# Performance work log

Hardware: AMD Instinct MI355X
Metric: run time of the kernel (lower is better)

Reference implementation:

```python
import jax, jax.numpy as jnp
import numpy as np

N = 64          # truth table size (2^6)
NUM_VARS = 6
TOP_K = 16
BATCH = 524288
IN_DIM = 17 + TOP_K  # 33
HID = 64
OUT = 64
EPS_LN = 1e-5


def _hadamard(n: int) -> np.ndarray:
    H = np.array([[1.0]], dtype=np.float32)
    while H.shape[0] < n:
        H = np.block([[H, H], [H, -H]])
    return H

_HAMMING = np.array([bin(i).count('1') for i in range(N)], dtype=np.float32)


def _xavier(key, fan_in, fan_out):
    lim = np.sqrt(6.0 / (fan_in + fan_out)).astype(np.float32)
    return jax.random.uniform(key, (fan_in, fan_out), jnp.float32, -lim, lim)


def setup_inputs() -> dict:
    key = jax.random.key(0)
    ks = jax.random.split(key, 4)
    truth_table = jax.random.randint(ks[0], (BATCH, N), 0, 2).astype(jnp.int32)
    H = jnp.asarray(_hadamard(N))
    return {
        'truth_table': truth_table,
        'H': H,
        'W1': _xavier(ks[1], IN_DIM, HID), 'b1': jnp.zeros((HID,), jnp.float32),
        'g1': jnp.ones((HID,), jnp.float32), 'be1': jnp.zeros((HID,), jnp.float32),
        'W2': _xavier(ks[2], HID, HID), 'b2': jnp.zeros((HID,), jnp.float32),
        'g2': jnp.ones((HID,), jnp.float32), 'be2': jnp.zeros((HID,), jnp.float32),
        'W3': _xavier(ks[3], HID, OUT), 'b3': jnp.zeros((OUT,), jnp.float32),
    }


def _layernorm(x, g, b):
    m = jnp.mean(x, axis=-1, keepdims=True)
    v = jnp.mean((x - m) ** 2, axis=-1, keepdims=True)
    return (x - m) / jnp.sqrt(v + EPS_LN) * g + b


def _walsh_features(truth_table, H):
    # Walsh-Hadamard transform: torch.mm(H, f.T).T == f @ H.T == f @ H (H symmetric)
    f_polar = 1.0 - 2.0 * truth_table.astype(jnp.float32)  # [B, 64]
    walsh = f_polar @ H                                     # [B, 64]
    walsh_abs = jnp.abs(walsh)
    walsh_sq = walsh * walsh
    n = jnp.float32(N)

    # --- key coefficients (8d): W(0), W(2^i) i=0..5, W(n-1) ---
    key_idx = jnp.array([0, 1, 2, 4, 8, 16, 32, N - 1])
    key_coeffs = walsh[:, key_idx] / n                      # [B, 8]

    # --- spectral statistics (5d) ---
    threshold = 0.1 * n
    sparsity = jnp.mean((walsh_abs < threshold).astype(jnp.float32), axis=1, keepdims=True)
    max_abs = jnp.max(walsh_abs, axis=1, keepdims=True)
    max_mag = max_abs / n
    l1 = jnp.sum(walsh_abs, axis=1, keepdims=True) / (n * n)
    sumsq = jnp.sum(walsh_sq, axis=1, keepdims=True)
    l2 = jnp.sqrt(sumsq) / (n * n)
    p = walsh_sq / (sumsq + 1e-10)
    entropy = -jnp.sum(p * jnp.log(p + 1e-10), axis=1, keepdims=True) / jnp.log(n)
    spectral = jnp.concatenate([sparsity, max_mag, l1, l2, entropy], axis=1)  # [B, 5]

    # --- linearity indicators (4d) ---
    large_coeffs = jnp.sum((walsh_abs > 0.5 * n).astype(jnp.float32), axis=1, keepdims=True)
    is_linear = ((large_coeffs >= 1) & (large_coeffs <= 2)).astype(jnp.float32)
    nonlinearity = jnp.clip(0.5 - max_abs / (2 * n), 0.0, 0.5) * 2.0
    hw = jnp.asarray(_HAMMING)
    large_mask = (walsh_abs > threshold).astype(jnp.float32)
    degree = jnp.sum(large_mask * hw, axis=1, keepdims=True) / (
        jnp.sum(large_mask, axis=1, keepdims=True) + 1e-10) / NUM_VARS
    bent_mag = jnp.float32(2.0 ** (NUM_VARS / 2))  # 8.0
    bent_dev = jnp.mean(jnp.abs(walsh_abs - bent_mag) / bent_mag, axis=1, keepdims=True)
    is_bent = (bent_dev < 0.1).astype(jnp.float32)
    linearity = jnp.concatenate([is_linear, nonlinearity, degree, is_bent], axis=1)  # [B, 4]

    # --- top-k |W| coefficients (16d) ---
    topk = jax.lax.top_k(walsh_abs, TOP_K)[0] / n            # [B, 16]

    return jnp.concatenate([key_coeffs, spectral, linearity, topk], axis=1)  # [B, 33]


def reference(truth_table, H, W1, b1, g1, be1, W2, b2, g2, be2, W3, b3):
    feats = _walsh_features(truth_table, H)
    h = jax.nn.gelu(_layernorm(feats @ W1 + b1, g1, be1), approximate=False)
    # Dropout(0.1) is identity in eval mode
    h = jax.nn.gelu(_layernorm(h @ W2 + b2, g2, be2), approximate=False)
    return h @ W3 + b3  # [B, 64]
```

## Files before the change

kernel.cpp:

```cpp
#include <hip/hip_runtime.h>
#include <math.h>

#define TPB 256

typedef _Float16 half8 __attribute__((ext_vector_type(8)));
typedef _Float16 h2 __attribute__((ext_vector_type(2)));
typedef float f32x4 __attribute__((ext_vector_type(4)));

__device__ __forceinline__ int swz(int row, int col) {
    return row * 64 + ((((col >> 3) ^ row) & 7) << 3) + (col & 7);
}

__device__ __forceinline__ unsigned int pk_f16(float a, float b) {
    auto p = __builtin_amdgcn_cvt_pkrtz(a, b);
    return __builtin_bit_cast(unsigned int, p);
}

__device__ __forceinline__ float gelu_sig(float x) {
    float t = fmaf(0.1029433247f, x * x, 2.3022089899f);
    float e = __builtin_amdgcn_exp2f(-x * t);
    return x * __builtin_amdgcn_rcpf(1.0f + e);
}

__device__ __forceinline__ void ce2(h2& x, h2& y) {
    h2 mx = __builtin_elementwise_max(x, y);
    h2 mn = __builtin_elementwise_min(x, y);
    x = mx; y = mn;
}

template<int CTRL>
__device__ __forceinline__ f32x4 dpp_add4(f32x4 x) {
#pragma unroll
    for (int r = 0; r < 4; ++r) {
        int o = __builtin_amdgcn_update_dpp(0, __float_as_int(x[r]),
                                            CTRL, 0xf, 0xf, false);
        x[r] += __int_as_float(o);
    }
    return x;
}
__device__ __forceinline__ f32x4 row_reduce16(f32x4 x) {
    x = dpp_add4<0x121>(x);
    x = dpp_add4<0x122>(x);
    x = dpp_add4<0x124>(x);
    x = dpp_add4<0x128>(x);
    return x;
}

__global__ void weight_stage_kernel(const float* __restrict__ W1,
                                    const float* __restrict__ W2,
                                    const float* __restrict__ W3,
                                    _Float16* __restrict__ wsW) {
    const int idx = blockIdx.x * 256 + threadIdx.x;
    if (idx >= 3 * 4 * 2 * 64 * 8) return;
    const int e    = idx & 7;
    const int lane = (idx >> 3) & 63;
    const int s    = (idx >> 9) & 1;
    const int nt   = (idx >> 10) & 3;
    const int L    = idx >> 12;
    const int g = lane >> 4, i = lane & 15;
    const int k = 32 * s + 8 * g + e;
    const int n = 4 * i + nt;
    const float* W = (L == 0) ? W1 : (L == 1) ? W2 : W3;
    const int K = (L == 0) ? 33 : 64;
    float val = (k < K) ? W[k * 64 + n] : 0.0f;
    if (L == 0 && (k < 8 || (k >= 17 && k < 33))) val *= 0.015625f;
    const _Float16 hi = (_Float16)val;
    const size_t base = ((((size_t)L * 4 + nt) * 2 + s) * 2) * 512
                        + (size_t)lane * 8 + e;
    wsW[base]       = hi;
    wsW[base + 512] = (_Float16)(val - (float)hi);
}

template<bool LAST>
__device__ __forceinline__ void mfma_layer(
    _Float16* actB,
    const _Float16* __restrict__ wsL,
    const float* __restrict__ bias, const float* __restrict__ gg,
    const float* __restrict__ bb,
    float* outp, int rowbase, int nrows)
{
    const int l = threadIdx.x & 63;
    const int g = l >> 4, i = l & 15;

    const half8* Bp = reinterpret_cast<const half8*>(wsL);
    half8 Bh[4][2], Bl[4][2];
#pragma unroll
    for (int nt = 0; nt < 4; ++nt) {
#pragma unroll
        for (int s = 0; s < 2; ++s) {
            Bh[nt][s] = Bp[((nt * 2 + s) * 2 + 0) * 64 + l];
            Bl[nt][s] = Bp[((nt * 2 + s) * 2 + 1) * 64 + l];
        }
    }
    const f32x4 bvv = *(const f32x4*)&bias[4 * i];
    f32x4 gvv, bevv;
    if (!LAST) {
        gvv  = *(const f32x4*)&gg[4 * i];
        bevv = *(const f32x4*)&bb[4 * i];
    }
    const bool full = LAST && (rowbase + 63 < nrows);

    half8 A0 = *(const half8*)&actB[swz(i, 8 * g)];
    half8 A1 = *(const half8*)&actB[swz(i, 32 + 8 * g)];

#pragma unroll
    for (int t = 0; t < 4; ++t) {
        half8 nA0, nA1;
        if (t < 3) {
            nA0 = *(const half8*)&actB[swz(16 * (t + 1) + i, 8 * g)];
            nA1 = *(const half8*)&actB[swz(16 * (t + 1) + i, 32 + 8 * g)];
        }
        f32x4 D[4];
#pragma unroll
        for (int nt = 0; nt < 4; ++nt) {
            f32x4 d = {bvv[nt], bvv[nt], bvv[nt], bvv[nt]};
            d = __builtin_amdgcn_mfma_f32_16x16x32_f16(A0, Bh[nt][0], d, 0, 0, 0);
            d = __builtin_amdgcn_mfma_f32_16x16x32_f16(A1, Bh[nt][1], d, 0, 0, 0);
            d = __builtin_amdgcn_mfma_f32_16x16x32_f16(A0, Bl[nt][0], d, 0, 0, 0);
            d = __builtin_amdgcn_mfma_f32_16x16x32_f16(A1, Bl[nt][1], d, 0, 0, 0);
            D[nt] = d;
        }
        if (LAST) {
#pragma unroll
            for (int r = 0; r < 4; ++r) {
                const int grow = rowbase + 16 * t + 4 * g + r;
                if (full || grow < nrows) {
                    f32x4 st = {D[0][r], D[1][r], D[2][r], D[3][r]};
                    *reinterpret_cast<f32x4*>(&outp[(size_t)grow * 64 + 4 * i]) = st;
                }
            }
        } else {
            f32x4 s4 = (D[0] + D[1]) + (D[2] + D[3]);
            f32x4 q4 = D[0] * D[0];
            q4 = D[1] * D[1] + q4;
            q4 = D[2] * D[2] + q4;
            q4 = D[3] * D[3] + q4;
            s4 = row_reduce16(s4);
            q4 = row_reduce16(q4);
            f32x4 mean = s4 * 0.015625f;
            f32x4 rstd, mr;
#pragma unroll
            for (int r = 0; r < 4; ++r) {
                float var = q4[r] * 0.015625f - mean[r] * mean[r];
                rstd[r] = rsqrtf(var + 1e-5f);
                mr[r] = -mean[r] * rstd[r];
            }
#pragma unroll
            for (int r = 0; r < 4; ++r) {
                float x0 = fmaf(fmaf(D[0][r], rstd[r], mr[r]), gvv[0], bevv[0]);
                float x1 = fmaf(fmaf(D[1][r], rstd[r], mr[r]), gvv[1], bevv[1]);
                float x2 = fmaf(fmaf(D[2][r], rstd[r], mr[r]), gvv[2], bevv[2]);
                float x3 = fmaf(fmaf(D[3][r], rstd[r], mr[r]), gvv[3], bevv[3]);
                uint2 st;
                st.x = pk_f16(gelu_sig(x0), gelu_sig(x1));
                st.y = pk_f16(gelu_sig(x2), gelu_sig(x3));
                *reinterpret_cast<uint2*>(
                    &actB[swz(16 * t + 4 * g + r, 4 * i)]) = st;
            }
        }
        if (t < 3) { A0 = nA0; A1 = nA1; }
    }
    if (!LAST) asm volatile("s_waitcnt lgkmcnt(0)" ::: "memory");
}

__global__ __launch_bounds__(TPB, 2) void walsh_mlp_kernel(
    const int* __restrict__ tt,
    const float* __restrict__ b1,
    const float* __restrict__ g1, const float* __restrict__ be1,
    const float* __restrict__ b2,
    const float* __restrict__ g2, const float* __restrict__ be2,
    const float* __restrict__ b3,
    const _Float16* __restrict__ wsW,
    float* __restrict__ out, int nrows)
{
    __shared__ __align__(16) _Float16 sAct[4][64][64];

    const int tid = threadIdx.x;
    const int w = tid >> 6, l = tid & 63;
    _Float16* actB = &sAct[w][0][0];

    const int row = blockIdx.x * TPB + tid;
    const int rowc = (row < nrows) ? row : (nrows - 1);

    int4 raw[16];
    const int4* t4 = reinterpret_cast<const int4*>(tt + (size_t)rowc * 64);
#pragma unroll
    for (int q = 0; q < 16; ++q) raw[q] = t4[q];

    {
        float* lut = reinterpret_cast<float*>(actB);
        if (l < 33) {
            const float a = 2.0f * (float)l;
            const float pq = (a * a) * 2.44140625e-4f;
            lut[l] = -(pq * __logf(pq + 1e-10f));
        }
    }
    asm volatile("s_waitcnt lgkmcnt(0)" ::: "memory");

    h2 p[32];
#pragma unroll
    for (int q = 0; q < 8; ++q) {
        int4 alo = raw[q];
        int4 ahi = raw[q + 8];
        p[4 * q + 0] = __builtin_bit_cast(h2,
            0x3C003C00u | ((unsigned)alo.x << 15) | ((unsigned)ahi.x << 31));
        p[4 * q + 1] = __builtin_bit_cast(h2,
            0x3C003C00u | ((unsigned)alo.y << 15) | ((unsigned)ahi.y << 31));
        p[4 * q + 2] = __builtin_bit_cast(h2,
            0x3C003C00u | ((unsigned)alo.z << 15) | ((unsigned)ahi.z << 31));
        p[4 * q + 3] = __builtin_bit_cast(h2,
            0x3C003C00u | ((unsigned)alo.w << 15) | ((unsigned)ahi.w << 31));
    }

#pragma unroll
    for (int h = 1; h < 32; h <<= 1) {
#pragma unroll
        for (int i = 0; i < 32; ++i) {
            if ((i & h) == 0) {
                h2 a = p[i], b = p[i | h];
                p[i] = a + b;
                p[i | h] = a - b;
            }
        }
    }

    const float inv_n = 1.0f / 64.0f;
    const float* lutr = reinterpret_cast<const float*>(actB);
    float f[17];
    h2 habs[32];
    const h2 kONE  = {(_Float16)1.0f, (_Float16)1.0f};
    const h2 kZERO = {(_Float16)0.0f, (_Float16)0.0f};
    const h2 k64   = {(_Float16)64.0f, (_Float16)64.0f};
    const h2 kCsp  = {(_Float16)409.5f, (_Float16)409.5f};
    const h2 kClg  = {(_Float16)-2080.0f, (_Float16)-2080.0f};
    const h2 kM8   = {(_Float16)-8.0f, (_Float16)-8.0f};
    h2 sum2 = kZERO, max2 = kZERO, bent2 = kZERO;
    h2 csp2 = kZERO, clg2 = kZERO, chw2 = kZERO;
    float ent = 0.0f;
#pragma unroll
    for (int i = 0; i < 32; ++i) {
        const float lo = (float)p[i][0], hi = (float)p[i][1];
        const float a0 = lo + hi;
        const float a1 = lo - hi;
        if (i == 0)  { f[0] = a0; f[6] = a1; }
        if (i == 1)  f[1] = a0;
        if (i == 2)  f[2] = a0;
        if (i == 4)  f[3] = a0;
        if (i == 8)  f[4] = a0;
        if (i == 16) f[5] = a0;
        if (i == 31) f[7] = a1;
        const h2 a = __builtin_bit_cast(h2, pk_f16(a0, a1) & 0x7FFF7FFFu);
        habs[i] = a;
        sum2 = sum2 + a;
        max2 = __builtin_elementwise_max(max2, a);
        bent2 = bent2 + __builtin_bit_cast(h2,
            __builtin_bit_cast(unsigned, a + kM8) & 0x7FFF7FFFu);
        const h2 ssp = __builtin_elementwise_min(kONE,
            __builtin_elementwise_max(kZERO, kCsp - a * k64));
        csp2 = csp2 + ssp;
        clg2 = clg2 + __builtin_elementwise_min(kONE,
            __builtin_elementwise_max(kZERO, a * k64 + kClg));
        const float PC = (float)__builtin_popcount(i);
        const h2 hp = {(_Float16)PC, (_Float16)PC};
        chw2 = chw2 + (kONE - ssp) * hp;
        ent += lutr[((int)fabsf(a0)) >> 1];
        ent += lutr[((int)fabsf(a1)) >> 1];
    }
    const float sumabs = (float)sum2[0] + (float)sum2[1];
    const float maxab  = fmaxf((float)max2[0], (float)max2[1]);
    const float bent   = (float)bent2[0] + (float)bent2[1];
    const float cnt_sp = (float)csp2[0] + (float)csp2[1];
    const float cnt_lg = (float)clg2[0] + (float)clg2[1];
    const float sum_hw = (float)chw2[0] + (float)chw2[1]
                       + (32.0f - (float)csp2[1]);

    f[8]  = cnt_sp * inv_n;
    f[9]  = maxab * inv_n;
    f[10] = sumabs * (1.0f / 4096.0f);
    f[11] = 0.015625f;
    f[12] = ent * 0.24044917348149316f;
    f[13] = (cnt_lg >= 0.5f && cnt_lg <= 2.5f) ? 1.0f : 0.0f;
    f[14] = fmaxf(0.0f, 0.5f - maxab * (1.0f / 128.0f)) * 2.0f;
    f[15] = sum_hw / (64.0f - cnt_sp + 1e-10f) * (1.0f / 6.0f);
    f[16] = (bent < 51.2f) ? 1.0f : 0.0f;

    h2 t2[16];
    {
#pragma unroll
        for (int base = 0; base < 32; base += 16) {
#pragma unroll
            for (int pp = 1; pp < 16; pp <<= 1) {
#pragma unroll
                for (int k = pp; k >= 1; k >>= 1) {
#pragma unroll
                    for (int j = k & (pp - 1); j + k < 16; j += 2 * k) {
#pragma unroll
                        for (int i = 0; i < k; ++i) {
                            if (i + j + k < 16 &&
                                (i + j) / (2 * pp) == (i + j + k) / (2 * pp))
                                ce2(habs[base + i + j], habs[base + i + j + k]);
                        }
                    }
                }
            }
        }
        h2 mm[16];
#pragma unroll
        for (int i = 0; i < 16; ++i)
            mm[i] = __builtin_elementwise_max(habs[i], habs[31 - i]);
#pragma unroll
        for (int d = 8; d >= 1; d >>= 1) {
#pragma unroll
            for (int i = 0; i < 16; ++i)
                if ((i & d) == 0) ce2(mm[i], mm[i + d]);
        }
#pragma unroll
        for (int i = 0; i < 16; ++i) {
            unsigned m = __builtin_bit_cast(unsigned, mm[15 - i]);
            unsigned sw = __builtin_amdgcn_alignbit(m, m, 16);
            t2[i] = __builtin_elementwise_max(mm[i], __builtin_bit_cast(h2, sw));
        }
#pragma unroll
        for (int d = 8; d >= 1; d >>= 1) {
#pragma unroll
            for (int i = 0; i < 16; ++i)
                if ((i & d) == 0) ce2(t2[i], t2[i + d]);
        }
    }

    {
        unsigned wd[32];
#pragma unroll
        for (int j = 0; j < 8; ++j) wd[j] = pk_f16(f[2 * j], f[2 * j + 1]);
        {
            unsigned lo = (unsigned)__builtin_bit_cast(unsigned short,
                                                       (_Float16)f[16]);
            wd[8] = lo | (__builtin_bit_cast(unsigned, t2[0]) << 16);
        }
#pragma unroll
        for (int m = 0; m < 7; ++m)
            wd[9 + m] = (__builtin_bit_cast(unsigned, t2[2 * m + 1]) & 0xFFFFu)
                      | (__builtin_bit_cast(unsigned, t2[2 * m + 2]) << 16);
        wd[16] = __builtin_bit_cast(unsigned, t2[15]) & 0xFFFFu;
#pragma unroll
        for (int j = 17; j < 32; ++j) wd[j] = 0u;
#pragma unroll
        for (int c = 0; c < 8; ++c) {
            uint4 st;
            st.x = wd[4 * c + 0]; st.y = wd[4 * c + 1];
            st.z = wd[4 * c + 2]; st.w = wd[4 * c + 3];
            *reinterpret_cast<uint4*>(&actB[swz(l, c * 8)]) = st;
        }
    }
    asm volatile("s_waitcnt lgkmcnt(0)" ::: "memory");

    const int rowbase = blockIdx.x * TPB + w * 64;
    mfma_layer<false>(actB, wsW,         b1, g1, be1, nullptr, 0, 0);
    mfma_layer<false>(actB, wsW + 8192,  b2, g2, be2, nullptr, 0, 0);
    mfma_layer<true >(actB, wsW + 16384, b3, nullptr, nullptr,
                      out, rowbase, nrows);
}

extern "C" void kernel_launch(void* const* d_in, const int* in_sizes, int n_in,
                              void* d_out, int out_size, void* d_ws, size_t ws_size,
                              hipStream_t stream) {
    const int*   tt  = (const int*)d_in[0];
    const float* W1  = (const float*)d_in[2];
    const float* b1  = (const float*)d_in[3];
    const float* g1  = (const float*)d_in[4];
    const float* be1 = (const float*)d_in[5];
    const float* W2  = (const float*)d_in[6];
    const float* b2  = (const float*)d_in[7];
    const float* g2  = (const float*)d_in[8];
    const float* be2 = (const float*)d_in[9];
    const float* W3  = (const float*)d_in[10];
    const float* b3  = (const float*)d_in[11];
    float* out = (float*)d_out;
    _Float16* wsW = (_Float16*)d_ws;

    const int nrows = in_sizes[0] / 64;

    hipLaunchKernelGGL(weight_stage_kernel, dim3(48), dim3(256), 0, stream,
                       W1, W2, W3, wsW);

    const int grid = (nrows + TPB - 1) / TPB;
    hipLaunchKernelGGL(walsh_mlp_kernel, dim3(grid), dim3(TPB), 0, stream,
                       tt, b1, g1, be1, b2, g2, be2, b3, wsW, out, nrows);
}
```

Measured before the change: 90.95 us.

## Use single-wave blocks, prefetch layer-1 weights, raise MFMA priority, interleave sort

Shrinks blocks from four waves to one, so each block uses a single 64x64 shared tile and the waves schedule independently. Loads the layer-1 high-half weight fragments early, before the feature store, to hide their global latency. Wraps the MFMA sequence in s_setprio to favour matrix issue, and interleaves the two 16-element sorting networks so there is more instruction-level parallelism. The risks are more blocks to launch and higher register pressure from the prefetched fragments.

Measured after the change: 86.88 us. -4.5%, faster.

```diff
diff --git a/kernel.cpp b/kernel.cpp
--- a/kernel.cpp
+++ b/kernel.cpp
@@ -1,7 +1,7 @@
 #include <hip/hip_runtime.h>
 #include <math.h>
 
-#define TPB 256
+#define TPB 64
 
 typedef _Float16 half8 __attribute__((ext_vector_type(8)));
 typedef _Float16 h2 __attribute__((ext_vector_type(2)));
@@ -75,6 +75,7 @@
 __device__ __forceinline__ void mfma_layer(
     _Float16* actB,
     const _Float16* __restrict__ wsL,
+    const half8 (*Bh_pre)[2],
     const float* __restrict__ bias, const float* __restrict__ gg,
     const float* __restrict__ bb,
     float* outp, int rowbase, int nrows)
@@ -88,7 +89,8 @@
     for (int nt = 0; nt < 4; ++nt) {
 #pragma unroll
         for (int s = 0; s < 2; ++s) {
-            Bh[nt][s] = Bp[((nt * 2 + s) * 2 + 0) * 64 + l];
+            Bh[nt][s] = Bh_pre ? Bh_pre[nt][s]
+                               : Bp[((nt * 2 + s) * 2 + 0) * 64 + l];
             Bl[nt][s] = Bp[((nt * 2 + s) * 2 + 1) * 64 + l];
         }
     }
@@ -111,6 +113,7 @@
             nA1 = *(const half8*)&actB[swz(16 * (t + 1) + i, 32 + 8 * g)];
         }
         f32x4 D[4];
+        __builtin_amdgcn_s_setprio(1);
 #pragma unroll
         for (int nt = 0; nt < 4; ++nt) {
             f32x4 d = {bvv[nt], bvv[nt], bvv[nt], bvv[nt]};
@@ -120,6 +123,7 @@
             d = __builtin_amdgcn_mfma_f32_16x16x32_f16(A1, Bl[nt][1], d, 0, 0, 0);
             D[nt] = d;
         }
+        __builtin_amdgcn_s_setprio(0);
         if (LAST) {
 #pragma unroll
             for (int r = 0; r < 4; ++r) {
@@ -173,11 +177,11 @@
     const _Float16* __restrict__ wsW,
     float* __restrict__ out, int nrows)
 {
-    __shared__ __align__(16) _Float16 sAct[4][64][64];
+    __shared__ __align__(16) _Float16 sAct[64][64];
 
     const int tid = threadIdx.x;
-    const int w = tid >> 6, l = tid & 63;
-    _Float16* actB = &sAct[w][0][0];
+    const int l = tid & 63;
+    _Float16* actB = &sAct[0][0];
 
     const int row = blockIdx.x * TPB + tid;
     const int rowc = (row < nrows) ? row : (nrows - 1);
@@ -287,18 +291,17 @@
     h2 t2[16];
     {
 #pragma unroll
-        for (int base = 0; base < 32; base += 16) {
-#pragma unroll
-            for (int pp = 1; pp < 16; pp <<= 1) {
-#pragma unroll
-                for (int k = pp; k >= 1; k >>= 1) {
-#pragma unroll
-                    for (int j = k & (pp - 1); j + k < 16; j += 2 * k) {
-#pragma unroll
-                        for (int i = 0; i < k; ++i) {
-                            if (i + j + k < 16 &&
-                                (i + j) / (2 * pp) == (i + j + k) / (2 * pp))
-                                ce2(habs[base + i + j], habs[base + i + j + k]);
+        for (int pp = 1; pp < 16; pp <<= 1) {
+#pragma unroll
+            for (int k = pp; k >= 1; k >>= 1) {
+#pragma unroll
+                for (int j = k & (pp - 1); j + k < 16; j += 2 * k) {
+#pragma unroll
+                    for (int i = 0; i < k; ++i) {
+                        if (i + j + k < 16 &&
+                            (i + j) / (2 * pp) == (i + j + k) / (2 * pp)) {
+                            ce2(habs[i + j],      habs[i + j + k]);
+                            ce2(habs[16 + i + j], habs[16 + i + j + k]);
                         }
                     }
                 }
@@ -326,6 +329,16 @@
             for (int i = 0; i < 16; ++i)
                 if ((i & d) == 0) ce2(t2[i], t2[i + d]);
         }
+    }
+
+    half8 B1h[4][2];
+    {
+        const half8* Bp1 = reinterpret_cast<const half8*>(wsW);
+#pragma unroll
+        for (int nt = 0; nt < 4; ++nt)
+#pragma unroll
+            for (int s = 0; s < 2; ++s)
+                B1h[nt][s] = Bp1[((nt * 2 + s) * 2 + 0) * 64 + l];
     }
 
     {
@@ -354,10 +367,12 @@
     }
     asm volatile("s_waitcnt lgkmcnt(0)" ::: "memory");
 
-    const int rowbase = blockIdx.x * TPB + w * 64;
-    mfma_layer<false>(actB, wsW,         b1, g1, be1, nullptr, 0, 0);
-    mfma_layer<false>(actB, wsW + 8192,  b2, g2, be2, nullptr, 0, 0);
-    mfma_layer<true >(actB, wsW + 16384, b3, nullptr, nullptr,
+    const int rowbase = blockIdx.x * TPB;
+    mfma_layer<false>(actB, wsW,         B1h,     b1, g1, be1,
+                      nullptr, 0, 0);
+    mfma_layer<false>(actB, wsW + 8192,  nullptr, b2, g2, be2,
+                      nullptr, 0, 0);
+    mfma_layer<true >(actB, wsW + 16384, nullptr, b3, nullptr, nullptr,
                       out, rowbase, nrows);
 }
 
```
